# Kernel tuning notes

Measured on AMD Instinct MI355X. Metric: run time of the kernel, lower is better.

## Reference

```python
import jax, jax.numpy as jnp
import numpy as np

ALPHA = 0.5      # GCN2Conv alpha
THETA = 1.0      # GCN2Conv theta (beta_l = log(theta/l + 1))
EPS = 1e-5       # pyg LayerNorm eps
N_LAYERS = 8
N, E, DIN, DHID, DOUT = 50000, 800000, 128, 256, 128


def setup_inputs() -> dict:
    key = jax.random.key(0)
    ks = jax.random.split(key, 10)
    x = jax.random.normal(ks[0], (N, DIN), jnp.float32)
    edge_index = jax.random.randint(ks[1], (2, E), 0, N, dtype=jnp.int32)
    lin1_w = jax.random.normal(ks[2], (DIN, DHID), jnp.float32) / np.sqrt(DIN)
    lin1_b = jnp.zeros((DHID,), jnp.float32)
    conv_w1 = jax.random.normal(ks[3], (N_LAYERS, DHID, DHID), jnp.float32) / np.sqrt(DHID)
    conv_w2 = jax.random.normal(ks[4], (N_LAYERS, DHID, DHID), jnp.float32) / np.sqrt(DHID)
    norm_gamma = jnp.ones((N_LAYERS, DHID), jnp.float32)
    norm_beta = jnp.zeros((N_LAYERS, DHID), jnp.float32)
    lin2_w = jax.random.normal(ks[5], (DHID, DOUT), jnp.float32) / np.sqrt(DHID)
    lin2_b = jnp.zeros((DOUT,), jnp.float32)
    return {"x": x, "edge_index": edge_index, "lin1_w": lin1_w, "lin1_b": lin1_b,
            "conv_w1": conv_w1, "conv_w2": conv_w2, "norm_gamma": norm_gamma,
            "norm_beta": norm_beta, "lin2_w": lin2_w, "lin2_b": lin2_b}


def _gcn_norm(edge_index, n_nodes, dtype):
    # add self loops, then symmetric deg^{-1/2} A_hat deg^{-1/2} normalization
    loop = jnp.arange(n_nodes, dtype=edge_index.dtype)
    row = jnp.concatenate([edge_index[0], loop])
    col = jnp.concatenate([edge_index[1], loop])
    deg = jax.ops.segment_sum(jnp.ones_like(row, dtype=dtype), col, num_segments=n_nodes)
    dis = jnp.where(deg > 0, jax.lax.rsqrt(jnp.maximum(deg, 1e-12)), 0.0)
    return row, col, dis[row] * dis[col]


def _graph_layernorm(h, gamma, beta):
    # pyg LayerNorm mode='graph', batch=None: normalize over all nodes+features
    z = h - jnp.mean(h)
    z = z / (jnp.sqrt(jnp.mean(z * z)) + EPS)
    return gamma * z + beta


def reference(x, edge_index, lin1_w, lin1_b, conv_w1, conv_w2, norm_gamma, norm_beta, lin2_w, lin2_b):
    n_nodes = x.shape[0]
    row, col, enorm = _gcn_norm(edge_index, n_nodes, x.dtype)
    # lin1 + relu (dropout p=0 -> identity); residual=None -> zeros
    x0 = jax.nn.relu(x @ lin1_w + lin1_b)
    h = x0
    for i in range(conv_w1.shape[0]):
        beta_l = float(np.log(THETA / (i + 1) + 1.0))
        # sparse neighborhood aggregation: out[c] += norm * h[r]
        agg = jax.ops.segment_sum(h[row] * enorm[:, None], col, num_segments=n_nodes)
        t = (1.0 - ALPHA) * agg          # propagated part
        r = ALPHA * x0                   # initial-residual part (res = x0 + zeros)
        # shared_weights=False: separate weights for propagated and residual parts
        h = (1.0 - beta_l) * (t + r) + beta_l * (t @ conv_w1[i] + r @ conv_w2[i])
        h = jax.nn.relu(_graph_layernorm(h, norm_gamma[i], norm_beta[i]))
    return jax.nn.relu(h @ lin2_w + lin2_b)
```

## Files before the change

### kernel.cpp

```cpp
#include <hip/hip_runtime.h>
#include <hip/hip_bf16.h>
#include <math.h>

#define DIN 128
#define DH 256
#define DOUT 128
#define NLAYERS 8
#define EPSLN 1e-5f

typedef __hip_bfloat16 bf16;
typedef __attribute__((ext_vector_type(8))) short short8;
typedef __attribute__((ext_vector_type(4))) short short4v;
typedef __attribute__((ext_vector_type(4))) float f32x4;

__device__ __forceinline__ float ldf(const void* p, size_t idx, int isbf) {
    if (isbf) return __bfloat162float(((const bf16*)p)[idx]);
    return ((const float*)p)[idx];
}
__device__ __forceinline__ short f2s(float v) {
    bf16 b = __float2bfloat16(v);
    return *reinterpret_cast<short*>(&b);
}
__device__ __forceinline__ float s2f(short s) {
    unsigned int u = ((unsigned int)(unsigned short)s) << 16;
    float f;
    __builtin_memcpy(&f, &u, 4);
    return f;
}
__device__ __forceinline__ void gl_lds16(const void* g, void* l) {
    __builtin_amdgcn_global_load_lds(
        (const __attribute__((address_space(1))) unsigned int*)g,
        (__attribute__((address_space(3))) unsigned int*)l,
        16, 0, 0);
}

__global__ void k_detect(const unsigned int* __restrict__ xw, int* __restrict__ flag) {
    __shared__ int cnt;
    if (threadIdx.x == 0) cnt = 0;
    __syncthreads();
    unsigned int w = xw[threadIdx.x];
    int e = (w >> 7) & 0xFF;
    if (e >= 112 && e <= 140) atomicAdd(&cnt, 1);
    __syncthreads();
    if (threadIdx.x == 0) *flag = (cnt >= 128) ? 1 : 0;
}

__global__ void k_init_cnt(int* __restrict__ cnt, int N) {
    int i = blockIdx.x * blockDim.x + threadIdx.x;
    if (i < N) cnt[i] = 0;
}
__global__ void k_count(const int* __restrict__ cols, int* __restrict__ cnt, int E) {
    int e = blockIdx.x * blockDim.x + threadIdx.x;
    if (e < E) atomicAdd(&cnt[cols[e]], 1);
}
__global__ void k_dis(const int* __restrict__ cnt, float* __restrict__ dis, int N) {
    int i = blockIdx.x * blockDim.x + threadIdx.x;
    if (i < N) dis[i] = rsqrtf(1.0f + (float)cnt[i]);
}
__global__ void k_scan1(const int* __restrict__ cnt, int* __restrict__ rowptr,
                        int* __restrict__ bsum, int N) {
    __shared__ int s[256];
    int t = threadIdx.x;
    int i = blockIdx.x * 256 + t;
    s[t] = (i < N) ? cnt[i] : 0;
    __syncthreads();
    for (int off = 1; off < 256; off <<= 1) {
        int x = (t >= off) ? s[t - off] : 0;
        __syncthreads();
        s[t] += x;
        __syncthreads();
    }
    if (i < N) rowptr[i + 1] = s[t];
    if (t == 255) bsum[blockIdx.x] = s[255];
}
__global__ void k_scan2(int* __restrict__ bsum, int nb) {
    __shared__ int s[256];
    int t = threadIdx.x;
    s[t] = (t < nb) ? bsum[t] : 0;
    __syncthreads();
    for (int off = 1; off < 256; off <<= 1) {
        int x = (t >= off) ? s[t - off] : 0;
        __syncthreads();
        s[t] += x;
        __syncthreads();
    }
    if (t < nb) bsum[t] = s[t];
}
__global__ void k_scan3(int* __restrict__ rowptr, const int* __restrict__ bsum, int N) {
    int i = blockIdx.x * 256 + threadIdx.x;
    if (i == 0) rowptr[0] = 0;
    if (i < N && blockIdx.x > 0) rowptr[i + 1] += bsum[blockIdx.x - 1];
}
__global__ void k_cursor(const int* __restrict__ rowptr, int* __restrict__ cursor, int N) {
    int i = blockIdx.x * 256 + threadIdx.x;
    if (i < N) cursor[i] = rowptr[i];
}
__global__ void k_fill(const int* __restrict__ rows, const int* __restrict__ cols,
                       int* __restrict__ cursor, int* __restrict__ csr, int E) {
    int e = blockIdx.x * blockDim.x + threadIdx.x;
    if (e < E) {
        int c = cols[e], r = rows[e];
        int pos = atomicAdd(&cursor[c], 1);
        csr[pos] = r;
    }
}

__global__ void k_zero_stats(float* __restrict__ stats) {
    int t = threadIdx.x;
    if (t < 16) stats[t] = 0.0f;
}

__global__ void k_transw2(const void* __restrict__ w1, const void* __restrict__ w2,
                          const int* __restrict__ flag, short* __restrict__ wt) {
    __shared__ float tile[32][33];
    int z = blockIdx.z;
    int lay = z >> 1, m = z & 1;
    const void* src = m ? w2 : w1;
    size_t sbase = (size_t)lay * 65536;
    short* dst = wt + (size_t)lay * 131072 + (size_t)m * 256;
    float bl = logf(1.0f / (float)(lay + 1) + 1.0f);
    float c0 = 0.5f * (1.0f - bl);
    float c1 = 0.5f * bl;
    int isbf = *flag;
    int tx = threadIdx.x, ty = threadIdx.y;
    int n0 = blockIdx.x * 32, k0 = blockIdx.y * 32;
    #pragma unroll
    for (int i = 0; i < 4; i++) {
        int k = k0 + ty + i * 8;
        tile[ty + i * 8][tx] = ldf(src, sbase + (size_t)k * 256 + n0 + tx, isbf);
    }
    __syncthreads();
    #pragma unroll
    for (int i = 0; i < 4; i++) {
        int n = n0 + ty + i * 8;
        int k = k0 + tx;
        float v = c1 * tile[tx][ty + i * 8];
        if (k == n) v += c0;
        dst[(size_t)n * 512 + k] = f2s(v);
    }
}

__global__ void k_transw_lin(const void* __restrict__ src, const int* __restrict__ flag,
                             short* __restrict__ dst, int K, int Nc) {
    __shared__ float tile[32][33];
    int isbf = *flag;
    int tx = threadIdx.x, ty = threadIdx.y;
    int n0 = blockIdx.x * 32, k0 = blockIdx.y * 32;
    #pragma unroll
    for (int i = 0; i < 4; i++) {
        int k = k0 + ty + i * 8;
        tile[ty + i * 8][tx] = ldf(src, (size_t)k * Nc + n0 + tx, isbf);
    }
    __syncthreads();
    #pragma unroll
    for (int i = 0; i < 4; i++) {
        int n = n0 + ty + i * 8;
        dst[(size_t)n * K + k0 + tx] = f2s(tile[tx][ty + i * 8]);
    }
}

__global__ void k_convx(const void* __restrict__ x, const int* __restrict__ flag,
                        short* __restrict__ xb, int total) {
    int i = blockIdx.x * 256 + threadIdx.x;
    if (i < total) xb[i] = f2s(ldf(x, i, *flag));
}

template<int BN, int KK, int FINAL>
__global__ __launch_bounds__(256) void gemm_mfma(
    const short* __restrict__ A, const short* __restrict__ wt,
    const void* __restrict__ bias, const int* __restrict__ flag,
    void* __restrict__ outp, int Nn)
{
    constexpr int NT = BN / 16;
    __shared__ __align__(16) short Atile[128 * 32];
    __shared__ __align__(16) short Btile[BN * 32];
    int t = threadIdx.x;
    int w = t >> 6, lane = t & 63;
    int lr = lane & 15, quad = lane >> 4;
    int row0 = blockIdx.x * 128;
    int sub = t & 3;
    int srow = t >> 2;
    f32x4 acc[2][NT];
    #pragma unroll
    for (int m = 0; m < 2; m++)
        #pragma unroll
        for (int nt = 0; nt < NT; nt++)
            #pragma unroll
            for (int j = 0; j < 4; j++) acc[m][nt][j] = 0.f;

    for (int kb = 0; kb < KK; kb += 32) {
        #pragma unroll
        for (int r = 0; r < 2; r++) {
            int gr = row0 + srow + r * 64;
            if (gr >= Nn) gr = Nn - 1;
            gl_lds16(A + (size_t)gr * KK + kb + sub * 8,
                     Atile + (size_t)(t + r * 256) * 8);
        }
        #pragma unroll
        for (int r = 0; r < BN / 64; r++) {
            int n = srow + r * 64;
            gl_lds16(wt + (size_t)n * KK + kb + sub * 8,
                     Btile + (size_t)(t + r * 256) * 8);
        }
        __syncthreads();
        short8 a0 = *(const short8*)(Atile + (w * 32 + lr) * 32 + quad * 8);
        short8 a1 = *(const short8*)(Atile + (w * 32 + 16 + lr) * 32 + quad * 8);
        #pragma unroll
        for (int nt = 0; nt < NT; nt++) {
            short8 bv = *(const short8*)(Btile + (nt * 16 + lr) * 32 + quad * 8);
            acc[0][nt] = __builtin_amdgcn_mfma_f32_16x16x32_bf16(a0, bv, acc[0][nt], 0, 0, 0);
            acc[1][nt] = __builtin_amdgcn_mfma_f32_16x16x32_bf16(a1, bv, acc[1][nt], 0, 0, 0);
        }
        __syncthreads();
    }
    const int isbf = *flag;
    #pragma unroll
    for (int m = 0; m < 2; m++) {
        #pragma unroll
        for (int nt = 0; nt < NT; nt++) {
            int gc = nt * 16 + lr;
            float bb = ldf(bias, gc, isbf);
            #pragma unroll
            for (int i = 0; i < 4; i++) {
                int gr = row0 + w * 32 + m * 16 + quad * 4 + i;
                if (gr < Nn) {
                    float v = acc[m][nt][i] + bb;
                    v = v > 0.f ? v : 0.f;
                    size_t off = (size_t)gr * BN + gc;
                    if (FINAL) {
                        if (isbf) ((bf16*)outp)[off] = __float2bfloat16(v);
                        else      ((float*)outp)[off] = v;
                    } else {
                        ((bf16*)outp)[off] = __float2bfloat16(v);
                    }
                }
            }
        }
    }
}

__global__ __launch_bounds__(256) void k_gather2(
    const int* __restrict__ rowptr, const int* __restrict__ csr,
    const float* __restrict__ dis, const bf16* __restrict__ hsrc,
    bf16* __restrict__ agg,
    const void* __restrict__ g, const void* __restrict__ b, size_t loff,
    const float* __restrict__ stats2, float invTotal, int useLN,
    const int* __restrict__ flag, int N)
{
    int gid = blockIdx.x * 256 + threadIdx.x;
    int node = gid >> 6;
    if (node >= N) return;
    int lane = gid & 63;
    int col = lane * 4;
    float cA[4], cB[4];
    if (useLN) {
        int isbf = *flag;
        float mu = stats2[0] * invTotal;
        float var = stats2[1] * invTotal - mu * mu;
        var = var > 0.f ? var : 0.f;
        float inv = 1.0f / (sqrtf(var) + EPSLN);
        #pragma unroll
        for (int j = 0; j < 4; j++) {
            float gg = ldf(g, loff + col + j, isbf);
            float bb = ldf(b, loff + col + j, isbf);
            cA[j] = gg * inv;
            cB[j] = fmaf(-gg * inv, mu, bb);
        }
    } else {
        #pragma unroll
        for (int j = 0; j < 4; j++) { cA[j] = 1.0f; cB[j] = 0.0f; }
    }
    const short* hs = (const short*)hsrc;
    float dc = dis[node];
    float acc[4], acc2[4];
    {
        short4v hv = *(const short4v*)(hs + (size_t)node * DH + col);
        #pragma unroll
        for (int j = 0; j < 4; j++) {
            float v = fmaf(cA[j], s2f(hv[j]), cB[j]);
            v = v > 0.f ? v : 0.f;
            acc[j] = dc * v;
            acc2[j] = 0.f;
        }
    }
    int i = rowptr[node], e1 = rowptr[node + 1];
    for (; i + 4 <= e1; i += 4) {
        int r0 = csr[i], r1 = csr[i + 1], r2 = csr[i + 2], r3 = csr[i + 3];
        float w0 = dis[r0], w1 = dis[r1], w2 = dis[r2], w3 = dis[r3];
        short4v v0 = *(const short4v*)(hs + (size_t)r0 * DH + col);
        short4v v1 = *(const short4v*)(hs + (size_t)r1 * DH + col);
        short4v v2 = *(const short4v*)(hs + (size_t)r2 * DH + col);
        short4v v3 = *(const short4v*)(hs + (size_t)r3 * DH + col);
        #pragma unroll
        for (int j = 0; j < 4; j++) {
            float a0 = fmaf(cA[j], s2f(v0[j]), cB[j]); a0 = a0 > 0.f ? a0 : 0.f;
            float a1 = fmaf(cA[j], s2f(v1[j]), cB[j]); a1 = a1 > 0.f ? a1 : 0.f;
            float a2 = fmaf(cA[j], s2f(v2[j]), cB[j]); a2 = a2 > 0.f ? a2 : 0.f;
            float a3 = fmaf(cA[j], s2f(v3[j]), cB[j]); a3 = a3 > 0.f ? a3 : 0.f;
            acc[j]  = fmaf(w0, a0, acc[j]);
            acc2[j] = fmaf(w1, a1, acc2[j]);
            acc[j]  = fmaf(w2, a2, acc[j]);
            acc2[j] = fmaf(w3, a3, acc2[j]);
        }
    }
    for (; i < e1; i++) {
        int r = csr[i];
        float wr = dis[r];
        short4v v0 = *(const short4v*)(hs + (size_t)r * DH + col);
        #pragma unroll
        for (int j = 0; j < 4; j++) {
            float a0 = fmaf(cA[j], s2f(v0[j]), cB[j]); a0 = a0 > 0.f ? a0 : 0.f;
            acc[j] = fmaf(wr, a0, acc[j]);
        }
    }
    short4v o;
    #pragma unroll
    for (int j = 0; j < 4; j++) o[j] = f2s(dc * (acc[j] + acc2[j]));
    *(short4v*)((short*)agg + (size_t)node * DH + col) = o;
}

__global__ __launch_bounds__(256) void gemm_layer3(
    const bf16* __restrict__ agg, const bf16* __restrict__ x0,
    const short* __restrict__ wt, bf16* __restrict__ h,
    float* __restrict__ stats2, int Nn)
{
    __shared__ __align__(16) short Atile[128 * 32];
    __shared__ __align__(16) short Btile[256 * 32];
    int t = threadIdx.x;
    int w = t >> 6, lane = t & 63;
    int lr = lane & 15, quad = lane >> 4;
    int row0 = blockIdx.x * 128;
    int sub = t & 3;
    int srow = t >> 2;
    f32x4 acc[2][16];
    #pragma unroll
    for (int m = 0; m < 2; m++)
        #pragma unroll
        for (int nt = 0; nt < 16; nt++)
            #pragma unroll
            for (int j = 0; j < 4; j++) acc[m][nt][j] = 0.f;

    for (int kb = 0; kb < 512; kb += 32) {
        const short* Asrc = (const short*)((kb < DH) ? agg : x0);
        int ka = kb & (DH - 1);
        #pragma unroll
        for (int r = 0; r < 2; r++) {
            int gr = row0 + srow + r * 64;
            if (gr >= Nn) gr = Nn - 1;
            gl_lds16(Asrc + (size_t)gr * DH + ka + sub * 8,
                     Atile + (size_t)(t + r * 256) * 8);
        }
        #pragma unroll
        for (int r = 0; r < 4; r++) {
            int n = srow + r * 64;
            gl_lds16(wt + (size_t)n * 512 + kb + sub * 8,
                     Btile + (size_t)(t + r * 256) * 8);
        }
        __syncthreads();
        short8 a0 = *(const short8*)(Atile + (w * 32 + lr) * 32 + quad * 8);
        short8 a1 = *(const short8*)(Atile + (w * 32 + 16 + lr) * 32 + quad * 8);
        #pragma unroll
        for (int nt = 0; nt < 16; nt++) {
            short8 bv = *(const short8*)(Btile + (nt * 16 + lr) * 32 + quad * 8);
            acc[0][nt] = __builtin_amdgcn_mfma_f32_16x16x32_bf16(a0, bv, acc[0][nt], 0, 0, 0);
            acc[1][nt] = __builtin_amdgcn_mfma_f32_16x16x32_bf16(a1, bv, acc[1][nt], 0, 0, 0);
        }
        __syncthreads();
    }
    float lsum = 0.f, lsq = 0.f;
    #pragma unroll
    for (int m = 0; m < 2; m++) {
        #pragma unroll
        for (int nt = 0; nt < 16; nt++) {
            int gc = nt * 16 + lr;
            #pragma unroll
            for (int i = 0; i < 4; i++) {
                int gr = row0 + w * 32 + m * 16 + quad * 4 + i;
                if (gr < Nn) {
                    float v = acc[m][nt][i];
                    h[(size_t)gr * DH + gc] = __float2bfloat16(v);
                    lsum += v;
                    lsq += v * v;
                }
            }
        }
    }
    float* red = (float*)Btile;
    red[t] = lsum;
    red[256 + t] = lsq;
    __syncthreads();
    for (int s = 128; s > 0; s >>= 1) {
        if (t < s) { red[t] += red[t + s]; red[256 + t] += red[256 + t + s]; }
        __syncthreads();
    }
    if (t == 0) {
        atomicAdd(&stats2[0], red[0]);
        atomicAdd(&stats2[1], red[256]);
    }
}

__global__ __launch_bounds__(256) void k_applyT(
    bf16* __restrict__ h, const float* __restrict__ stats2, float invTotal,
    const void* __restrict__ g, const void* __restrict__ b, size_t loff,
    const int* __restrict__ flag, int total)
{
    int idx = blockIdx.x * 256 + threadIdx.x;
    if (idx >= total) return;
    const int isbf = *flag;
    float mu = stats2[0] * invTotal;
    float var = stats2[1] * invTotal - mu * mu;
    var = var > 0.f ? var : 0.f;
    float inv = 1.0f / (sqrtf(var) + EPSLN);
    int j = idx & (DH - 1);
    float gg = ldf(g, loff + j, isbf);
    float bb = ldf(b, loff + j, isbf);
    float v = fmaf(gg * inv, __bfloat162float(h[idx]), fmaf(-gg * inv, mu, bb));
    v = v > 0.f ? v : 0.f;
    h[idx] = __float2bfloat16(v);
}

extern "C" void kernel_launch(void* const* d_in, const int* in_sizes, int n_in,
                              void* d_out, int out_size, void* d_ws, size_t ws_size,
                              hipStream_t stream) {
    const void* x      = d_in[0];
    const int*  ei     = (const int*)d_in[1];
    const void* lin1_w = d_in[2];
    const void* lin1_b = d_in[3];
    const void* conv_w1= d_in[4];
    const void* conv_w2= d_in[5];
    const void* gam    = d_in[6];
    const void* bet    = d_in[7];
    const void* lin2_w = d_in[8];
    const void* lin2_b = d_in[9];

    const int N = in_sizes[0] / DIN;
    const int E = in_sizes[1] / 2;
    const int* rows = ei;
    const int* cols = ei + E;
    const size_t NDH = (size_t)N * DH;
    const size_t Nr = ((size_t)N + 255) / 256 * 256;

    char* p = (char*)d_ws;
    auto alloc = [&](size_t bytes) { char* q = p; p += (bytes + 255) & ~(size_t)255; return q; };
    float* dis    = (float*)alloc(Nr * 4);
    float* stats  = (float*)alloc(1024);
    int*   flag   = (int*)(stats + 16);
    int*   cnt    = (int*)alloc(Nr * 4);
    int*   rowptr = (int*)alloc((Nr + 256) * 4);
    int*   cursor = (int*)alloc(Nr * 4);
    int*   bsum   = (int*)alloc(1024);
    int*   csr    = (int*)alloc((size_t)E * 4);
    short* wt     = (short*)alloc((size_t)NLAYERS * 131072 * 2);
    short* w1t    = (short*)alloc((size_t)DH * DIN * 2);
    short* w2t    = (short*)alloc((size_t)DOUT * DH * 2);
    short* xb     = (short*)alloc((size_t)N * DIN * 2);
    bf16*  agg    = (bf16*)alloc(NDH * 2);
    bf16*  x0     = (bf16*)alloc(NDH * 2);
    bf16*  h      = (bf16*)alloc(NDH * 2);

    dim3 blk(256);
    int nbN = (N + 255) / 256;
    dim3 gN(nbN);
    dim3 gE((E + 255) / 256);
    dim3 gB((N + 127) / 128);
    dim3 gG((N + 3) / 4);
    dim3 gElem((unsigned)((NDH + 255) / 256));
    dim3 gTW(8, 8, 16);
    dim3 bTW(32, 8);

    k_detect<<<1, 256, 0, stream>>>((const unsigned int*)x, flag);
    k_init_cnt<<<gN, blk, 0, stream>>>(cnt, N);
    k_count<<<gE, blk, 0, stream>>>(cols, cnt, E);
    k_dis<<<gN, blk, 0, stream>>>(cnt, dis, N);
    k_scan1<<<gN, blk, 0, stream>>>(cnt, rowptr, bsum, N);
    k_scan2<<<1, 256, 0, stream>>>(bsum, nbN);
    k_scan3<<<gN, blk, 0, stream>>>(rowptr, bsum, N);
    k_cursor<<<gN, blk, 0, stream>>>(rowptr, cursor, N);
    k_fill<<<gE, blk, 0, stream>>>(rows, cols, cursor, csr, E);
    k_zero_stats<<<1, 64, 0, stream>>>(stats);
    k_transw2<<<gTW, bTW, 0, stream>>>(conv_w1, conv_w2, flag, wt);
    k_transw_lin<<<dim3(DH / 32, DIN / 32), bTW, 0, stream>>>(lin1_w, flag, w1t, DIN, DH);
    k_transw_lin<<<dim3(DOUT / 32, DH / 32), bTW, 0, stream>>>(lin2_w, flag, w2t, DH, DOUT);
    k_convx<<<dim3((unsigned)(((size_t)N * DIN + 255) / 256)), blk, 0, stream>>>(x, flag, xb, N * DIN);

    gemm_mfma<DH, DIN, 0><<<gB, blk, 0, stream>>>(xb, w1t, lin1_b, flag, x0, N);

    const float invTotal = 1.0f / ((float)N * (float)DH);
    for (int l = 0; l < NLAYERS; l++) {
        const bf16* hsrc = (l == 0) ? x0 : h;
        size_t loff = (l == 0) ? 0 : (size_t)(l - 1) * DH;
        const float* st = (l == 0) ? stats : stats + 2 * (l - 1);
        k_gather2<<<gG, blk, 0, stream>>>(rowptr, csr, dis, hsrc, agg,
                                          gam, bet, loff, st, invTotal,
                                          l > 0 ? 1 : 0, flag, N);
        gemm_layer3<<<gB, blk, 0, stream>>>(agg, x0, wt + (size_t)l * 131072,
                                            h, stats + 2 * l, N);
    }
    k_applyT<<<gElem, blk, 0, stream>>>(h, stats + 2 * (NLAYERS - 1), invTotal,
                                        gam, bet, (size_t)(NLAYERS - 1) * DH,
                                        flag, (int)NDH);
    gemm_mfma<DOUT, DH, 1><<<gB, blk, 0, stream>>>((const short*)h, w2t, lin2_b,
                                                   flag, d_out, N);
}
```

Before: 1.276 ms.

## Split GEMM output columns across grid and pack two nodes per wave in gather

The GEMMs now tile the output as 128x128 blocks with a second grid dimension over columns, which halves the per-block accumulator and B-tile footprint and doubles the block count. This aims to raise occupancy and parallelism, at the cost of re-reading the A rows once per column block. The gather kernel now handles two nodes per wave with 8-element (16-byte) loads per lane, giving wider memory transactions and more nodes in flight per wave. Its unroll drops from 4 edges to 2, and the LayerNorm reduction buffer moves into its own shared array.

```diff
diff --git a/kernel.cpp b/kernel.cpp
--- a/kernel.cpp
+++ b/kernel.cpp
@@ -10,7 +10,6 @@
 
 typedef __hip_bfloat16 bf16;
 typedef __attribute__((ext_vector_type(8))) short short8;
-typedef __attribute__((ext_vector_type(4))) short short4v;
 typedef __attribute__((ext_vector_type(4))) float f32x4;
 
 __device__ __forceinline__ float ldf(const void* p, size_t idx, int isbf) {
@@ -165,26 +164,27 @@
     if (i < total) xb[i] = f2s(ldf(x, i, *flag));
 }
 
-template<int BN, int KK, int FINAL>
+template<int KK, int FINAL>
 __global__ __launch_bounds__(256) void gemm_mfma(
     const short* __restrict__ A, const short* __restrict__ wt,
     const void* __restrict__ bias, const int* __restrict__ flag,
     void* __restrict__ outp, int Nn)
 {
-    constexpr int NT = BN / 16;
     __shared__ __align__(16) short Atile[128 * 32];
-    __shared__ __align__(16) short Btile[BN * 32];
+    __shared__ __align__(16) short Btile[128 * 32];
     int t = threadIdx.x;
     int w = t >> 6, lane = t & 63;
     int lr = lane & 15, quad = lane >> 4;
     int row0 = blockIdx.x * 128;
+    int col0 = blockIdx.y * 128;
+    int ncols = gridDim.y * 128;
     int sub = t & 3;
     int srow = t >> 2;
-    f32x4 acc[2][NT];
+    f32x4 acc[2][8];
     #pragma unroll
     for (int m = 0; m < 2; m++)
         #pragma unroll
-        for (int nt = 0; nt < NT; nt++)
+        for (int nt = 0; nt < 8; nt++)
             #pragma unroll
             for (int j = 0; j < 4; j++) acc[m][nt][j] = 0.f;
 
@@ -197,8 +197,8 @@
                      Atile + (size_t)(t + r * 256) * 8);
         }
         #pragma unroll
-        for (int r = 0; r < BN / 64; r++) {
-            int n = srow + r * 64;
+        for (int r = 0; r < 2; r++) {
+            int n = col0 + srow + r * 64;
             gl_lds16(wt + (size_t)n * KK + kb + sub * 8,
                      Btile + (size_t)(t + r * 256) * 8);
         }
@@ -206,7 +206,7 @@
         short8 a0 = *(const short8*)(Atile + (w * 32 + lr) * 32 + quad * 8);
         short8 a1 = *(const short8*)(Atile + (w * 32 + 16 + lr) * 32 + quad * 8);
         #pragma unroll
-        for (int nt = 0; nt < NT; nt++) {
+        for (int nt = 0; nt < 8; nt++) {
             short8 bv = *(const short8*)(Btile + (nt * 16 + lr) * 32 + quad * 8);
             acc[0][nt] = __builtin_amdgcn_mfma_f32_16x16x32_bf16(a0, bv, acc[0][nt], 0, 0, 0);
             acc[1][nt] = __builtin_amdgcn_mfma_f32_16x16x32_bf16(a1, bv, acc[1][nt], 0, 0, 0);
@@ -217,8 +217,8 @@
     #pragma unroll
     for (int m = 0; m < 2; m++) {
         #pragma unroll
-        for (int nt = 0; nt < NT; nt++) {
-            int gc = nt * 16 + lr;
+        for (int nt = 0; nt < 8; nt++) {
+            int gc = col0 + nt * 16 + lr;
             float bb = ldf(bias, gc, isbf);
             #pragma unroll
             for (int i = 0; i < 4; i++) {
@@ -226,7 +226,7 @@
                 if (gr < Nn) {
                     float v = acc[m][nt][i] + bb;
                     v = v > 0.f ? v : 0.f;
-                    size_t off = (size_t)gr * BN + gc;
+                    size_t off = (size_t)gr * ncols + gc;
                     if (FINAL) {
                         if (isbf) ((bf16*)outp)[off] = __float2bfloat16(v);
                         else      ((float*)outp)[off] = v;
@@ -239,7 +239,7 @@
     }
 }
 
-__global__ __launch_bounds__(256) void k_gather2(
+__global__ __launch_bounds__(256) void k_gather3(
     const int* __restrict__ rowptr, const int* __restrict__ csr,
     const float* __restrict__ dis, const bf16* __restrict__ hsrc,
     bf16* __restrict__ agg,
@@ -247,12 +247,15 @@
     const float* __restrict__ stats2, float invTotal, int useLN,
     const int* __restrict__ flag, int N)
 {
-    int gid = blockIdx.x * 256 + threadIdx.x;
-    int node = gid >> 6;
-    if (node >= N) return;
-    int lane = gid & 63;
-    int col = lane * 4;
-    float cA[4], cB[4];
+    int t = threadIdx.x;
+    int wave = t >> 6, lane = t & 63;
+    int half = lane >> 5;
+    int sl = lane & 31;
+    int node = blockIdx.x * 8 + wave * 2 + half;
+    bool ok = node < N;
+    if (!ok) node = N - 1;
+    int col = sl * 8;
+    float cA[8], cB[8];
     if (useLN) {
         int isbf = *flag;
         float mu = stats2[0] * invTotal;
@@ -260,7 +263,7 @@
         var = var > 0.f ? var : 0.f;
         float inv = 1.0f / (sqrtf(var) + EPSLN);
         #pragma unroll
-        for (int j = 0; j < 4; j++) {
+        for (int j = 0; j < 8; j++) {
             float gg = ldf(g, loff + col + j, isbf);
             float bb = ldf(b, loff + col + j, isbf);
             cA[j] = gg * inv;
@@ -268,75 +271,72 @@
         }
     } else {
         #pragma unroll
-        for (int j = 0; j < 4; j++) { cA[j] = 1.0f; cB[j] = 0.0f; }
+        for (int j = 0; j < 8; j++) { cA[j] = 1.0f; cB[j] = 0.0f; }
     }
     const short* hs = (const short*)hsrc;
     float dc = dis[node];
-    float acc[4], acc2[4];
+    float acc[8];
     {
-        short4v hv = *(const short4v*)(hs + (size_t)node * DH + col);
-        #pragma unroll
-        for (int j = 0; j < 4; j++) {
+        short8 hv = *(const short8*)(hs + (size_t)node * DH + col);
+        #pragma unroll
+        for (int j = 0; j < 8; j++) {
             float v = fmaf(cA[j], s2f(hv[j]), cB[j]);
             v = v > 0.f ? v : 0.f;
             acc[j] = dc * v;
-            acc2[j] = 0.f;
         }
     }
     int i = rowptr[node], e1 = rowptr[node + 1];
-    for (; i + 4 <= e1; i += 4) {
-        int r0 = csr[i], r1 = csr[i + 1], r2 = csr[i + 2], r3 = csr[i + 3];
-        float w0 = dis[r0], w1 = dis[r1], w2 = dis[r2], w3 = dis[r3];
-        short4v v0 = *(const short4v*)(hs + (size_t)r0 * DH + col);
-        short4v v1 = *(const short4v*)(hs + (size_t)r1 * DH + col);
-        short4v v2 = *(const short4v*)(hs + (size_t)r2 * DH + col);
-        short4v v3 = *(const short4v*)(hs + (size_t)r3 * DH + col);
-        #pragma unroll
-        for (int j = 0; j < 4; j++) {
+    for (; i + 2 <= e1; i += 2) {
+        int r0 = csr[i], r1 = csr[i + 1];
+        float w0 = dis[r0], w1 = dis[r1];
+        short8 v0 = *(const short8*)(hs + (size_t)r0 * DH + col);
+        short8 v1 = *(const short8*)(hs + (size_t)r1 * DH + col);
+        #pragma unroll
+        for (int j = 0; j < 8; j++) {
             float a0 = fmaf(cA[j], s2f(v0[j]), cB[j]); a0 = a0 > 0.f ? a0 : 0.f;
             float a1 = fmaf(cA[j], s2f(v1[j]), cB[j]); a1 = a1 > 0.f ? a1 : 0.f;
-            float a2 = fmaf(cA[j], s2f(v2[j]), cB[j]); a2 = a2 > 0.f ? a2 : 0.f;
-            float a3 = fmaf(cA[j], s2f(v3[j]), cB[j]); a3 = a3 > 0.f ? a3 : 0.f;
-            acc[j]  = fmaf(w0, a0, acc[j]);
-            acc2[j] = fmaf(w1, a1, acc2[j]);
-            acc[j]  = fmaf(w2, a2, acc[j]);
-            acc2[j] = fmaf(w3, a3, acc2[j]);
+            acc[j] = fmaf(w0, a0, acc[j]);
+            acc[j] = fmaf(w1, a1, acc[j]);
         }
     }
     for (; i < e1; i++) {
         int r = csr[i];
         float wr = dis[r];
-        short4v v0 = *(const short4v*)(hs + (size_t)r * DH + col);
-        #pragma unroll
-        for (int j = 0; j < 4; j++) {
+        short8 v0 = *(const short8*)(hs + (size_t)r * DH + col);
+        #pragma unroll
+        for (int j = 0; j < 8; j++) {
             float a0 = fmaf(cA[j], s2f(v0[j]), cB[j]); a0 = a0 > 0.f ? a0 : 0.f;
             acc[j] = fmaf(wr, a0, acc[j]);
         }
     }
-    short4v o;
-    #pragma unroll
-    for (int j = 0; j < 4; j++) o[j] = f2s(dc * (acc[j] + acc2[j]));
-    *(short4v*)((short*)agg + (size_t)node * DH + col) = o;
-}
-
-__global__ __launch_bounds__(256) void gemm_layer3(
+    if (ok) {
+        short8 o;
+        #pragma unroll
+        for (int j = 0; j < 8; j++) o[j] = f2s(dc * acc[j]);
+        *(short8*)((short*)agg + (size_t)node * DH + col) = o;
+    }
+}
+
+__global__ __launch_bounds__(256) void gemm_layer4(
     const bf16* __restrict__ agg, const bf16* __restrict__ x0,
     const short* __restrict__ wt, bf16* __restrict__ h,
     float* __restrict__ stats2, int Nn)
 {
     __shared__ __align__(16) short Atile[128 * 32];
-    __shared__ __align__(16) short Btile[256 * 32];
+    __shared__ __align__(16) short Btile[128 * 32];
+    __shared__ float red[512];
     int t = threadIdx.x;
     int w = t >> 6, lane = t & 63;
     int lr = lane & 15, quad = lane >> 4;
     int row0 = blockIdx.x * 128;
+    int col0 = blockIdx.y * 128;
     int sub = t & 3;
     int srow = t >> 2;
-    f32x4 acc[2][16];
+    f32x4 acc[2][8];
     #pragma unroll
     for (int m = 0; m < 2; m++)
         #pragma unroll
-        for (int nt = 0; nt < 16; nt++)
+        for (int nt = 0; nt < 8; nt++)
             #pragma unroll
             for (int j = 0; j < 4; j++) acc[m][nt][j] = 0.f;
 
@@ -351,8 +351,8 @@
                      Atile + (size_t)(t + r * 256) * 8);
         }
         #pragma unroll
-        for (int r = 0; r < 4; r++) {
-            int n = srow + r * 64;
+        for (int r = 0; r < 2; r++) {
+            int n = col0 + srow + r * 64;
             gl_lds16(wt + (size_t)n * 512 + kb + sub * 8,
                      Btile + (size_t)(t + r * 256) * 8);
         }
@@ -360,7 +360,7 @@
         short8 a0 = *(const short8*)(Atile + (w * 32 + lr) * 32 + quad * 8);
         short8 a1 = *(const short8*)(Atile + (w * 32 + 16 + lr) * 32 + quad * 8);
         #pragma unroll
-        for (int nt = 0; nt < 16; nt++) {
+        for (int nt = 0; nt < 8; nt++) {
             short8 bv = *(const short8*)(Btile + (nt * 16 + lr) * 32 + quad * 8);
             acc[0][nt] = __builtin_amdgcn_mfma_f32_16x16x32_bf16(a0, bv, acc[0][nt], 0, 0, 0);
             acc[1][nt] = __builtin_amdgcn_mfma_f32_16x16x32_bf16(a1, bv, acc[1][nt], 0, 0, 0);
@@ -371,8 +371,8 @@
     #pragma unroll
     for (int m = 0; m < 2; m++) {
         #pragma unroll
-        for (int nt = 0; nt < 16; nt++) {
-            int gc = nt * 16 + lr;
+        for (int nt = 0; nt < 8; nt++) {
+            int gc = col0 + nt * 16 + lr;
             #pragma unroll
             for (int i = 0; i < 4; i++) {
                 int gr = row0 + w * 32 + m * 16 + quad * 4 + i;
@@ -385,7 +385,6 @@
             }
         }
     }
-    float* red = (float*)Btile;
     red[t] = lsum;
     red[256 + t] = lsq;
     __syncthreads();
@@ -462,8 +461,9 @@
     int nbN = (N + 255) / 256;
     dim3 gN(nbN);
     dim3 gE((E + 255) / 256);
-    dim3 gB((N + 127) / 128);
-    dim3 gG((N + 3) / 4);
+    dim3 gB128_2((N + 127) / 128, 2);
+    dim3 gB128_1((N + 127) / 128, 1);
+    dim3 gG((N + 7) / 8);
     dim3 gElem((unsigned)((NDH + 255) / 256));
     dim3 gTW(8, 8, 16);
     dim3 bTW(32, 8);
@@ -483,22 +483,22 @@
     k_transw_lin<<<dim3(DOUT / 32, DH / 32), bTW, 0, stream>>>(lin2_w, flag, w2t, DH, DOUT);
     k_convx<<<dim3((unsigned)(((size_t)N * DIN + 255) / 256)), blk, 0, stream>>>(x, flag, xb, N * DIN);
 
-    gemm_mfma<DH, DIN, 0><<<gB, blk, 0, stream>>>(xb, w1t, lin1_b, flag, x0, N);
+    gemm_mfma<DIN, 0><<<gB128_2, blk, 0, stream>>>(xb, w1t, lin1_b, flag, x0, N);
 
     const float invTotal = 1.0f / ((float)N * (float)DH);
     for (int l = 0; l < NLAYERS; l++) {
         const bf16* hsrc = (l == 0) ? x0 : h;
         size_t loff = (l == 0) ? 0 : (size_t)(l - 1) * DH;
         const float* st = (l == 0) ? stats : stats + 2 * (l - 1);
-        k_gather2<<<gG, blk, 0, stream>>>(rowptr, csr, dis, hsrc, agg,
+        k_gather3<<<gG, blk, 0, stream>>>(rowptr, csr, dis, hsrc, agg,
                                           gam, bet, loff, st, invTotal,
                                           l > 0 ? 1 : 0, flag, N);
-        gemm_layer3<<<gB, blk, 0, stream>>>(agg, x0, wt + (size_t)l * 131072,
-                                            h, stats + 2 * l, N);
+        gemm_layer4<<<gB128_2, blk, 0, stream>>>(agg, x0, wt + (size_t)l * 131072,
+                                                 h, stats + 2 * l, N);
     }
     k_applyT<<<gElem, blk, 0, stream>>>(h, stats + 2 * (NLAYERS - 1), invTotal,
                                         gam, bet, (size_t)(NLAYERS - 1) * DH,
                                         flag, (int)NDH);
-    gemm_mfma<DOUT, DH, 1><<<gB, blk, 0, stream>>>((const short*)h, w2t, lin2_b,
-                                                   flag, d_out, N);
-}
+    gemm_mfma<DH, 1><<<gB128_1, blk, 0, stream>>>((const short*)h, w2t, lin2_b,
+                                                  flag, d_out, N);
+}
```

Measured after the change: 1.339 ms. +4.9%, slower.
